# Optimization experiments

Hardware: AMD Instinct MI355X
Metric: run time of the kernel (lower is better)

The kernel has to match this reference:

```python
import jax, jax.numpy as jnp
import numpy as np

B, S, D = 2, 2048, 1024
H = 16
HD = D // H

def setup_inputs() -> dict:
    key = jax.random.key(0)
    ks = jax.random.split(key, 9)
    s = 1.0 / np.sqrt(D)
    return {
        "x": jax.random.normal(ks[0], (B, S, D), dtype=jnp.float32),
        "Wq": jax.random.normal(ks[1], (D, D), dtype=jnp.float32) * s,
        "bq": jnp.zeros((D,), dtype=jnp.float32),
        "Wk": jax.random.normal(ks[2], (D, D), dtype=jnp.float32) * s,
        "bk": jnp.zeros((D,), dtype=jnp.float32),
        "Wv": jax.random.normal(ks[3], (D, D), dtype=jnp.float32) * s,
        "bv": jnp.zeros((D,), dtype=jnp.float32),
        "Wo": jax.random.normal(ks[4], (D, D), dtype=jnp.float32) * s,
        "bo": jnp.zeros((D,), dtype=jnp.float32),
    }

def reference(x, Wq, bq, Wk, bk, Wv, bv, Wo, bo):
    b, s, d = x.shape
    # torch Linear: y = x @ W.T + b
    def proj(W, bias):
        y = jnp.einsum('bsd,ed->bse', x, W) + bias
        return y.reshape(b, s, H, HD).transpose(0, 2, 1, 3)  # [b,h,s,hd]
    Q = proj(Wq, bq)
    K = proj(Wk, bk)
    V = proj(Wv, bv)
    scale = 1.0 / jnp.sqrt(jnp.float32(HD))
    scores = jnp.einsum('bhqd,bhkd->bhqk', Q, K) * scale  # [b,h,s,s]
    attn = jax.nn.softmax(scores, axis=-1)
    out = jnp.einsum('bhqk,bhkd->bhqd', attn, V)  # [b,h,s,hd]
    out = out.transpose(0, 2, 1, 3).reshape(b, s, d)
    return jnp.einsum('bsd,ed->bse', out, Wo) + bo
```

## Files before the change

### kernel.cpp

```cpp
#include <hip/hip_runtime.h>
#include <stdint.h>


typedef __bf16 bf16x8 __attribute__((ext_vector_type(8)));
typedef float  f32x4  __attribute__((ext_vector_type(4)));

#define LOG2E 1.44269504088896f
#define FIXED_MAX_BITS 14.4269504088896f

__device__ __forceinline__ unsigned short f2bf(float f) {
    union { float f; unsigned u; } v; v.f = f;
    unsigned r = v.u + 0x7FFFu + ((v.u >> 16) & 1u);
    return (unsigned short)(r >> 16);
}
__device__ __forceinline__ float bf2f(unsigned short u) {
    union { unsigned u; float f; } v; v.u = (unsigned)u << 16; return v.f;
}

__device__ __forceinline__ float exp2_fast(float x) {
#if __has_builtin(__builtin_amdgcn_exp2f)
    return __builtin_amdgcn_exp2f(x);
#else
    return __expf(x * 0.69314718056f);
#endif
}

__device__ __forceinline__ void glds16(const void* g, void* l) {
    __builtin_amdgcn_global_load_lds(
        (__attribute__((address_space(1))) void*)(g),
        (__attribute__((address_space(3))) void*)(l),
        16, 0, 0);
}

__global__ __launch_bounds__(256) void cvt_all(
    const float* __restrict__ x,  const float* __restrict__ Wq,
    const float* __restrict__ Wk, const float* __restrict__ Wv,
    const float* __restrict__ Wo,
    unsigned short* __restrict__ xb,  unsigned short* __restrict__ Wqb,
    unsigned short* __restrict__ Wkb, unsigned short* __restrict__ Wvb,
    unsigned short* __restrict__ Wob)
{
    const int stride = gridDim.x * blockDim.x;
    for (int i = blockIdx.x * blockDim.x + threadIdx.x; i < 2097152; i += stride) {
        const float* src; unsigned short* dst; int j;
        if (i < 1048576) { src = x; dst = xb; j = i; }
        else {
            int t = (i - 1048576) >> 18; j = (i - 1048576) & 262143;
            src = (t == 0) ? Wq : (t == 1) ? Wk : (t == 2) ? Wv : Wo;
            dst = (t == 0) ? Wqb : (t == 1) ? Wkb : (t == 2) ? Wvb : Wob;
        }
        float4 v = ((const float4*)src)[j];
        ushort4 o;
        o.x = f2bf(v.x); o.y = f2bf(v.y); o.z = f2bf(v.z); o.w = f2bf(v.w);
        ((ushort4*)dst)[j] = o;
    }
}

template <int MODE>
__global__ __launch_bounds__(256) void gemm_bt(
    const unsigned short* __restrict__ A,
    const unsigned short* __restrict__ W0,
    const unsigned short* __restrict__ W1,
    const unsigned short* __restrict__ W2,
    const float* __restrict__ b0,
    const float* __restrict__ b1,
    const float* __restrict__ b2,
    unsigned short* __restrict__ outQ,
    unsigned short* __restrict__ outK,
    unsigned short* __restrict__ outV,
    float* __restrict__ outF)
{
    constexpr int BM = (MODE == 0) ? 128 : 64;
    constexpr int FM = BM / 32;
    constexpr int RA = BM / 32;

    __shared__ __attribute__((aligned(16))) unsigned short As[2 * BM * 64];
    __shared__ __attribute__((aligned(16))) unsigned short Bs[2 * 128 * 64];

    const int tid  = threadIdx.x;
    const int lane = tid & 63;
    const int wid  = tid >> 6;
    const int quad = lane >> 4;
    const int l16  = lane & 15;

    const int m0 = blockIdx.x * BM;

    const unsigned short* W;
    const float* bias;
    int proj, n0;
    if (MODE == 0) {
        proj = blockIdx.y >> 3;
        n0   = (blockIdx.y & 7) * 128;
        W    = (proj == 0) ? W0 : (proj == 1) ? W1 : W2;
        bias = (proj == 0) ? b0 : (proj == 1) ? b1 : b2;
    } else {
        proj = 0;
        n0   = blockIdx.y * 128;
        W    = W0;
        bias = b0;
    }

    const int wm = (wid >> 1) * (BM / 2);
    const int wn = (wid & 1) * 64;

    f32x4 acc[FM][4];
#pragma unroll
    for (int i = 0; i < FM; ++i)
#pragma unroll
        for (int j = 0; j < 4; ++j)
            acc[i][j] = (f32x4){0.f, 0.f, 0.f, 0.f};

    char* AsB = (char*)As;
    char* BsB = (char*)Bs;

    auto stageAB = [&](int k0, int buf) {
        char* ldsA = AsB + buf * (BM * 128) + wid * 1024;
        char* ldsB = BsB + buf * 16384 + wid * 1024;
#pragma unroll
        for (int q = 0; q < RA; ++q) {
            int i   = q * 256 + tid;
            int row = i >> 3;
            int sc  = (i & 7) ^ (row & 7);
            glds16(A + (size_t)(m0 + row) * 1024 + k0 + sc * 8, ldsA + q * 4096);
        }
#pragma unroll
        for (int q = 0; q < 4; ++q) {
            int i   = q * 256 + tid;
            int row = i >> 3;
            int sc  = (i & 7) ^ (row & 7);
            glds16(W + (size_t)(n0 + row) * 1024 + k0 + sc * 8, ldsB + q * 4096);
        }
    };

    stageAB(0, 0);
    __syncthreads();

    for (int k0 = 0; k0 < 1024; k0 += 64) {
        const int cur = (k0 >> 6) & 1;
        if (k0 + 64 < 1024) stageAB(k0 + 64, cur ^ 1);

        const char* AsC = AsB + cur * (BM * 128);
        const char* BsC = BsB + cur * 16384;

#pragma unroll
        for (int kh = 0; kh < 2; ++kh) {
            bf16x8 af[FM], bfr[4];
#pragma unroll
            for (int t = 0; t < FM; ++t) {
                int r = wm + t * 16 + l16;
                int c = (kh * 4 + quad) ^ (r & 7);
                af[t] = *(const bf16x8*)(AsC + r * 128 + c * 16);
            }
#pragma unroll
            for (int t = 0; t < 4; ++t) {
                int r = wn + t * 16 + l16;
                int c = (kh * 4 + quad) ^ (r & 7);
                bfr[t] = *(const bf16x8*)(BsC + r * 128 + c * 16);
            }
#pragma unroll
            for (int i = 0; i < FM; ++i)
#pragma unroll
                for (int j = 0; j < 4; ++j)
                    acc[i][j] = __builtin_amdgcn_mfma_f32_16x16x32_bf16(
                        af[i], bfr[j], acc[i][j], 0, 0, 0);
        }
        __syncthreads();
    }

#pragma unroll
    for (int i = 0; i < FM; ++i) {
        const int mrow0 = m0 + wm + i * 16 + quad * 4;
#pragma unroll
        for (int j = 0; j < 4; ++j) {
            const int n  = n0 + wn + j * 16 + l16;
            const float bb = bias[n];
            if (MODE == 1) {
#pragma unroll
                for (int r = 0; r < 4; ++r)
                    outF[(size_t)(mrow0 + r) * 1024 + n] = acc[i][j][r] + bb;
            } else {
                const int h = n >> 6, hd = n & 63;
                if (proj == 2) {
                    const int b = mrow0 >> 11, s = mrow0 & 2047;
                    ushort4 pk;
                    pk.x = f2bf(acc[i][j][0] + bb);
                    pk.y = f2bf(acc[i][j][1] + bb);
                    pk.z = f2bf(acc[i][j][2] + bb);
                    pk.w = f2bf(acc[i][j][3] + bb);
                    *(ushort4*)(outV + ((size_t)((b * 16 + h) * 64 + hd)) * 2048 + s) = pk;
                } else {
                    unsigned short* dst = (proj == 0) ? outQ : outK;
                    const float scl = (proj == 0) ? (0.125f * LOG2E) : 1.0f;
#pragma unroll
                    for (int r = 0; r < 4; ++r) {
                        const int m = mrow0 + r;
                        const int b = m >> 11, s = m & 2047;
                        dst[((size_t)((b * 16 + h) * 2048 + s)) * 64 + hd] =
                            f2bf((acc[i][j][r] + bb) * scl);
                    }
                }
            }
        }
    }
}

__global__ __launch_bounds__(256, 4) void attn_kernel(
    const unsigned short* __restrict__ Qb,
    const unsigned short* __restrict__ Kb,
    const unsigned short* __restrict__ Vtb,
    unsigned short* __restrict__ OP,
    float* __restrict__ LS)
{
    __shared__ __attribute__((aligned(16))) unsigned short Ks[2 * 64 * 64];
    __shared__ __attribute__((aligned(16))) unsigned short Vs[2 * 64 * 64];

    const int tid  = threadIdx.x;
    const int lane = tid & 63;
    const int wid  = tid >> 6;
    const int quad = lane >> 4;
    const int l16  = lane & 15;
    const int l7   = l16 & 7;

    const int bid  = blockIdx.x + (blockIdx.y << 5);
    const int c8   = bid & 7;
    const int t    = bid >> 3;
    const int hb   = c8 + ((t >> 5) << 3);
    const int u    = t & 31;
    const int qt16 = u >> 1;
    const int half = u & 1;
    const int q0   = qt16 * 128 + wid * 32;
    const int bq   = hb >> 4, hh = hb & 15;

    const unsigned short* Qh  = Qb  + (size_t)hb * 2048 * 64;
    const unsigned short* Kh  = Kb  + (size_t)hb * 2048 * 64;
    const unsigned short* Vth = Vtb + (size_t)hb * 64 * 2048;

    bf16x8 qf[2][2];
#pragma unroll
    for (int qt = 0; qt < 2; ++qt) {
        const unsigned short* qp = Qh + (size_t)(q0 + qt * 16 + l16) * 64 + quad * 8;
        qf[qt][0] = *(const bf16x8*)(qp);
        qf[qt][1] = *(const bf16x8*)(qp + 32);
    }

    f32x4 o[4][2];
#pragma unroll
    for (int ht = 0; ht < 4; ++ht)
#pragma unroll
        for (int qt = 0; qt < 2; ++qt)
            o[ht][qt] = (f32x4){0.f, 0.f, 0.f, 0.f};
    float lsum[2] = {0.f, 0.f};

    char* KsB = (char*)Ks;
    char* VsB = (char*)Vs;

    auto stageKV = [&](int kc, int buf) {
        char* ldsK = KsB + buf * 8192 + wid * 1024;
#pragma unroll
        for (int q = 0; q < 2; ++q) {
            int i   = q * 256 + tid;
            int row = i >> 3;
            int g   = (row & 3) | (((row >> 3) & 1) << 2);
            int ch  = (i & 7) ^ g;
            glds16(Kh + (size_t)(kc + row) * 64 + ch * 8, ldsK + q * 4096);
        }
        char* ldsV = VsB + buf * 8192 + wid * 1024;
#pragma unroll
        for (int q = 0; q < 2; ++q) {
            int i   = q * 256 + tid;
            int row = i >> 3;
            int ch  = (i & 7) ^ (row & 7);
            glds16(Vth + (size_t)row * 2048 + kc + ch * 8, ldsV + q * 4096);
        }
    };

    const int base_row = 8 * (l16 >> 2) + (l16 & 3);
    const int kp0 = ((quad) ^ l7) * 16;
    const int kp1 = ((4 + quad) ^ l7) * 16;
    const int vrow = l16 * 128;

    const int kc0 = half * 1024;
    stageKV(kc0, 0);
    __syncthreads();

    for (int kc = kc0; kc < kc0 + 1024; kc += 64) {
        const int cur = (kc >> 6) & 1;
        if (kc + 64 < kc0 + 1024) stageKV(kc + 64, cur ^ 1);

        const char* KsC = KsB + cur * 8192;
        const char* VsC = VsB + cur * 8192;

#pragma unroll
        for (int st32 = 0; st32 < 2; ++st32) {
            const char* krb = KsC + (st32 * 32 + base_row) * 128;
            bf16x8 kf00 = *(const bf16x8*)(krb + kp0);
            bf16x8 kf01 = *(const bf16x8*)(krb + kp1);
            bf16x8 kf10 = *(const bf16x8*)(krb + 512 + kp0);
            bf16x8 kf11 = *(const bf16x8*)(krb + 512 + kp1);

            const f32x4 mi = (f32x4){-FIXED_MAX_BITS, -FIXED_MAX_BITS,
                                     -FIXED_MAX_BITS, -FIXED_MAX_BITS};
            f32x4 s00 = mi, s01 = mi, s10 = mi, s11 = mi;
            s00 = __builtin_amdgcn_mfma_f32_16x16x32_bf16(kf00, qf[0][0], s00, 0, 0, 0);
            s00 = __builtin_amdgcn_mfma_f32_16x16x32_bf16(kf01, qf[0][1], s00, 0, 0, 0);
            s01 = __builtin_amdgcn_mfma_f32_16x16x32_bf16(kf10, qf[0][0], s01, 0, 0, 0);
            s01 = __builtin_amdgcn_mfma_f32_16x16x32_bf16(kf11, qf[0][1], s01, 0, 0, 0);
            s10 = __builtin_amdgcn_mfma_f32_16x16x32_bf16(kf00, qf[1][0], s10, 0, 0, 0);
            s10 = __builtin_amdgcn_mfma_f32_16x16x32_bf16(kf01, qf[1][1], s10, 0, 0, 0);
            s11 = __builtin_amdgcn_mfma_f32_16x16x32_bf16(kf10, qf[1][0], s11, 0, 0, 0);
            s11 = __builtin_amdgcn_mfma_f32_16x16x32_bf16(kf11, qf[1][1], s11, 0, 0, 0);

            bf16x8 p8[2];
#pragma unroll
            for (int qt = 0; qt < 2; ++qt) {
                const f32x4 sA = qt ? s10 : s00;
                const f32x4 sB = qt ? s11 : s01;
                float e0 = exp2_fast(sA[0]), e1 = exp2_fast(sA[1]);
                float e2 = exp2_fast(sA[2]), e3 = exp2_fast(sA[3]);
                float e4 = exp2_fast(sB[0]), e5 = exp2_fast(sB[1]);
                float e6 = exp2_fast(sB[2]), e7 = exp2_fast(sB[3]);
                lsum[qt] += ((e0 + e1) + (e2 + e3)) + ((e4 + e5) + (e6 + e7));
                bf16x8 p;
                p[0] = (__bf16)e0; p[1] = (__bf16)e1;
                p[2] = (__bf16)e2; p[3] = (__bf16)e3;
                p[4] = (__bf16)e4; p[5] = (__bf16)e5;
                p[6] = (__bf16)e6; p[7] = (__bf16)e7;
                p8[qt] = p;
            }

            const int voff = vrow + (((st32 * 4 + quad) ^ l7) * 16);
#pragma unroll
            for (int ht = 0; ht < 4; ++ht) {
                const bf16x8 vf = *(const bf16x8*)(VsC + voff + ht * 2048);
                o[ht][0] = __builtin_amdgcn_mfma_f32_16x16x32_bf16(vf, p8[0], o[ht][0], 0, 0, 0);
                o[ht][1] = __builtin_amdgcn_mfma_f32_16x16x32_bf16(vf, p8[1], o[ht][1], 0, 0, 0);
            }
        }
        __syncthreads();
    }

    float lt[2];
#pragma unroll
    for (int qt = 0; qt < 2; ++qt) {
        float s = lsum[qt];
        s += __shfl_xor(s, 16);
        s += __shfl_xor(s, 32);
        lt[qt] = s;
    }

    unsigned short* OPh = OP + (size_t)half * 4096 * 1024;
#pragma unroll
    for (int qt = 0; qt < 2; ++qt) {
        const size_t row = (size_t)(bq * 2048 + q0 + qt * 16 + l16);
#pragma unroll
        for (int ht = 0; ht < 4; ++ht) {
            ushort4 pk;
            pk.x = f2bf(o[ht][qt][0]);
            pk.y = f2bf(o[ht][qt][1]);
            pk.z = f2bf(o[ht][qt][2]);
            pk.w = f2bf(o[ht][qt][3]);
            *(ushort4*)(OPh + row * 1024 + hh * 64 + ht * 16 + quad * 4) = pk;
        }
    }
    if (quad == 0) {
        LS[half * 65536 + hb * 2048 + q0 + l16]      = lt[0];
        LS[half * 65536 + hb * 2048 + q0 + 16 + l16] = lt[1];
    }
}

__global__ __launch_bounds__(256) void attn_reduce(
    const unsigned short* __restrict__ OP,
    const float* __restrict__ LS,
    unsigned short* __restrict__ attnb)
{
    const size_t idx = ((size_t)blockIdx.x * 256 + threadIdx.x) * 8;
    const int row = (int)(idx >> 10);
    const int col = (int)(idx & 1023);
    const int bh  = ((row >> 11) << 4) + (col >> 6);
    const int q   = row & 2047;
    const float l = LS[bh * 2048 + q] + LS[65536 + bh * 2048 + q];
    const float rl = 1.0f / l;

    ushort4 a0 = *(const ushort4*)(OP + idx);
    ushort4 a1 = *(const ushort4*)(OP + idx + 4);
    ushort4 b0 = *(const ushort4*)(OP + 4194304 + idx);
    ushort4 b1 = *(const ushort4*)(OP + 4194304 + idx + 4);
    ushort4 o0, o1;
    o0.x = f2bf((bf2f(a0.x) + bf2f(b0.x)) * rl);
    o0.y = f2bf((bf2f(a0.y) + bf2f(b0.y)) * rl);
    o0.z = f2bf((bf2f(a0.z) + bf2f(b0.z)) * rl);
    o0.w = f2bf((bf2f(a0.w) + bf2f(b0.w)) * rl);
    o1.x = f2bf((bf2f(a1.x) + bf2f(b1.x)) * rl);
    o1.y = f2bf((bf2f(a1.y) + bf2f(b1.y)) * rl);
    o1.z = f2bf((bf2f(a1.z) + bf2f(b1.z)) * rl);
    o1.w = f2bf((bf2f(a1.w) + bf2f(b1.w)) * rl);
    *(ushort4*)(attnb + idx)     = o0;
    *(ushort4*)(attnb + idx + 4) = o1;
}

extern "C" void kernel_launch(void* const* d_in, const int* in_sizes, int n_in,
                              void* d_out, int out_size, void* d_ws, size_t ws_size,
                              hipStream_t stream) {
    (void)in_sizes; (void)n_in; (void)out_size; (void)ws_size;

    const float* x  = (const float*)d_in[0];
    const float* Wq = (const float*)d_in[1];
    const float* bq = (const float*)d_in[2];
    const float* Wk = (const float*)d_in[3];
    const float* bk = (const float*)d_in[4];
    const float* Wv = (const float*)d_in[5];
    const float* bv = (const float*)d_in[6];
    const float* Wo = (const float*)d_in[7];
    const float* bo = (const float*)d_in[8];

    char* ws = (char*)d_ws;
    const size_t MB = 1024 * 1024;
    unsigned short* xb    = (unsigned short*)(ws + 0);
    unsigned short* Wqb   = (unsigned short*)(ws + 8  * MB);
    unsigned short* Wkb   = (unsigned short*)(ws + 10 * MB);
    unsigned short* Wvb   = (unsigned short*)(ws + 12 * MB);
    unsigned short* Wob   = (unsigned short*)(ws + 14 * MB);
    unsigned short* Qb    = (unsigned short*)(ws + 16 * MB);
    unsigned short* Kb    = (unsigned short*)(ws + 24 * MB);
    unsigned short* Vtb   = (unsigned short*)(ws + 32 * MB);
    unsigned short* attnb = (unsigned short*)(ws + 40 * MB);
    unsigned short* OP    = (unsigned short*)(ws + 48 * MB);
    float*          LSb   = (float*)(ws + 64 * MB);

    cvt_all<<<dim3(1024), dim3(256), 0, stream>>>(
        x, Wq, Wk, Wv, Wo, xb, Wqb, Wkb, Wvb, Wob);

    gemm_bt<0><<<dim3(32, 24), dim3(256), 0, stream>>>(
        xb, Wqb, Wkb, Wvb, bq, bk, bv, Qb, Kb, Vtb, nullptr);

    attn_kernel<<<dim3(32, 32), dim3(256), 0, stream>>>(Qb, Kb, Vtb, OP, LSb);

    attn_reduce<<<dim3(2048), dim3(256), 0, stream>>>(OP, LSb, attnb);

    gemm_bt<1><<<dim3(64, 8), dim3(256), 0, stream>>>(
        attnb, Wob, nullptr, nullptr, bo, nullptr, nullptr,
        nullptr, nullptr, nullptr, (float*)d_out);
}
```

Baseline: 189.8 us.

## Fuse split-KV attention reduce into output projection GEMM A-tile loading

Removes the separate attn_reduce kernel. The output-projection GEMM now loads both partial attention outputs into registers, sums them, scales by a per-row reciprocal of the summed softmax denominators kept in shared memory, and writes bf16 into the LDS A tile, with the commit placed after the MFMAs. This drops one kernel launch and a full write and reread of the combined attention buffer. In exchange the GEMM reads twice the A data through registers instead of async global-to-LDS loads, and register pressure rises. The attention kernel's launch-bounds occupancy hint is also raised from 4 to 5.

```diff
diff --git a/kernel.cpp b/kernel.cpp
--- a/kernel.cpp
+++ b/kernel.cpp
@@ -12,9 +12,6 @@
     union { float f; unsigned u; } v; v.f = f;
     unsigned r = v.u + 0x7FFFu + ((v.u >> 16) & 1u);
     return (unsigned short)(r >> 16);
-}
-__device__ __forceinline__ float bf2f(unsigned short u) {
-    union { unsigned u; float f; } v; v.u = (unsigned)u << 16; return v.f;
 }
 
 __device__ __forceinline__ float exp2_fast(float x) {
@@ -23,6 +20,18 @@
 #else
     return __expf(x * 0.69314718056f);
 #endif
+}
+
+__device__ __forceinline__ unsigned comb2(unsigned wa, unsigned wb, float rl) {
+    union { unsigned u; float f; } la, ha, lb, hb;
+    la.u = wa << 16; ha.u = wa & 0xffff0000u;
+    lb.u = wb << 16; hb.u = wb & 0xffff0000u;
+    float lo = (la.f + lb.f) * rl;
+    float hi = (ha.f + hb.f) * rl;
+    __bf16 l = (__bf16)lo, h = (__bf16)hi;
+    unsigned short lu = __builtin_bit_cast(unsigned short, l);
+    unsigned short hu = __builtin_bit_cast(unsigned short, h);
+    return (unsigned)lu | ((unsigned)hu << 16);
 }
 
 __device__ __forceinline__ void glds16(const void* g, void* l) {
@@ -76,6 +85,7 @@
 
     __shared__ __attribute__((aligned(16))) unsigned short As[2 * BM * 64];
     __shared__ __attribute__((aligned(16))) unsigned short Bs[2 * 128 * 64];
+    __shared__ float Lrec[(MODE == 1) ? 1024 : 4];
 
     const int tid  = threadIdx.x;
     const int lane = tid & 63;
@@ -113,9 +123,18 @@
     char* AsB = (char*)As;
     char* BsB = (char*)Bs;
 
-    auto stageAB = [&](int k0, int buf) {
+    auto stageB = [&](int k0, int buf) {
+        char* ldsB = BsB + buf * 16384 + wid * 1024;
+#pragma unroll
+        for (int q = 0; q < 4; ++q) {
+            int i   = q * 256 + tid;
+            int row = i >> 3;
+            int sc  = (i & 7) ^ (row & 7);
+            glds16(W + (size_t)(n0 + row) * 1024 + k0 + sc * 8, ldsB + q * 4096);
+        }
+    };
+    auto stageA_g = [&](int k0, int buf) {
         char* ldsA = AsB + buf * (BM * 128) + wid * 1024;
-        char* ldsB = BsB + buf * 16384 + wid * 1024;
 #pragma unroll
         for (int q = 0; q < RA; ++q) {
             int i   = q * 256 + tid;
@@ -123,21 +142,68 @@
             int sc  = (i & 7) ^ (row & 7);
             glds16(A + (size_t)(m0 + row) * 1024 + k0 + sc * 8, ldsA + q * 4096);
         }
-#pragma unroll
-        for (int q = 0; q < 4; ++q) {
+    };
+
+    uint4 ar0[2], ar1[2];
+    float arl[2];
+    auto aload = [&](int k0) {
+#pragma unroll
+        for (int q = 0; q < 2; ++q) {
             int i   = q * 256 + tid;
             int row = i >> 3;
             int sc  = (i & 7) ^ (row & 7);
-            glds16(W + (size_t)(n0 + row) * 1024 + k0 + sc * 8, ldsB + q * 4096);
+            const size_t gof = (size_t)(m0 + row) * 1024 + k0 + sc * 8;
+            ar0[q] = *(const uint4*)(A + gof);
+            ar1[q] = *(const uint4*)(A + 4194304 + gof);
+            arl[q] = Lrec[row * 16 + (k0 >> 6)];
         }
     };
-
-    stageAB(0, 0);
+    auto acommit = [&](int buf) {
+#pragma unroll
+        for (int q = 0; q < 2; ++q) {
+            int i = q * 256 + tid;
+            uint4 o;
+            o.x = comb2(ar0[q].x, ar1[q].x, arl[q]);
+            o.y = comb2(ar0[q].y, ar1[q].y, arl[q]);
+            o.z = comb2(ar0[q].z, ar1[q].z, arl[q]);
+            o.w = comb2(ar0[q].w, ar1[q].w, arl[q]);
+            *(uint4*)(AsB + buf * (BM * 128) + i * 16) = o;
+        }
+    };
+
+    if constexpr (MODE == 1) {
+        const float* LSp = b1;
+        const int bq16 = (m0 >> 11) << 4;
+        const int mq0  = m0 & 2047;
+#pragma unroll
+        for (int j = 0; j < 4; ++j) {
+            int idx = j * 256 + tid;
+            int rr  = idx >> 4, h = idx & 15;
+            int off = (bq16 + h) * 2048 + mq0 + rr;
+            Lrec[idx] = 1.0f / (LSp[off] + LSp[65536 + off]);
+        }
+        __syncthreads();
+        aload(0);
+        acommit(0);
+        stageB(0, 0);
+    } else {
+        stageA_g(0, 0);
+        stageB(0, 0);
+    }
     __syncthreads();
 
     for (int k0 = 0; k0 < 1024; k0 += 64) {
         const int cur = (k0 >> 6) & 1;
-        if (k0 + 64 < 1024) stageAB(k0 + 64, cur ^ 1);
+        const bool pf = (k0 + 64 < 1024);
+        if (pf) {
+            if constexpr (MODE == 1) {
+                aload(k0 + 64);
+                stageB(k0 + 64, cur ^ 1);
+            } else {
+                stageA_g(k0 + 64, cur ^ 1);
+                stageB(k0 + 64, cur ^ 1);
+            }
+        }
 
         const char* AsC = AsB + cur * (BM * 128);
         const char* BsC = BsB + cur * 16384;
@@ -163,6 +229,10 @@
                 for (int j = 0; j < 4; ++j)
                     acc[i][j] = __builtin_amdgcn_mfma_f32_16x16x32_bf16(
                         af[i], bfr[j], acc[i][j], 0, 0, 0);
+        }
+
+        if constexpr (MODE == 1) {
+            if (pf) acommit(cur ^ 1);
         }
         __syncthreads();
     }
@@ -204,7 +274,7 @@
     }
 }
 
-__global__ __launch_bounds__(256, 4) void attn_kernel(
+__global__ __launch_bounds__(256, 5) void attn_kernel(
     const unsigned short* __restrict__ Qb,
     const unsigned short* __restrict__ Kb,
     const unsigned short* __restrict__ Vtb,
@@ -368,36 +438,6 @@
     }
 }
 
-__global__ __launch_bounds__(256) void attn_reduce(
-    const unsigned short* __restrict__ OP,
-    const float* __restrict__ LS,
-    unsigned short* __restrict__ attnb)
-{
-    const size_t idx = ((size_t)blockIdx.x * 256 + threadIdx.x) * 8;
-    const int row = (int)(idx >> 10);
-    const int col = (int)(idx & 1023);
-    const int bh  = ((row >> 11) << 4) + (col >> 6);
-    const int q   = row & 2047;
-    const float l = LS[bh * 2048 + q] + LS[65536 + bh * 2048 + q];
-    const float rl = 1.0f / l;
-
-    ushort4 a0 = *(const ushort4*)(OP + idx);
-    ushort4 a1 = *(const ushort4*)(OP + idx + 4);
-    ushort4 b0 = *(const ushort4*)(OP + 4194304 + idx);
-    ushort4 b1 = *(const ushort4*)(OP + 4194304 + idx + 4);
-    ushort4 o0, o1;
-    o0.x = f2bf((bf2f(a0.x) + bf2f(b0.x)) * rl);
-    o0.y = f2bf((bf2f(a0.y) + bf2f(b0.y)) * rl);
-    o0.z = f2bf((bf2f(a0.z) + bf2f(b0.z)) * rl);
-    o0.w = f2bf((bf2f(a0.w) + bf2f(b0.w)) * rl);
-    o1.x = f2bf((bf2f(a1.x) + bf2f(b1.x)) * rl);
-    o1.y = f2bf((bf2f(a1.y) + bf2f(b1.y)) * rl);
-    o1.z = f2bf((bf2f(a1.z) + bf2f(b1.z)) * rl);
-    o1.w = f2bf((bf2f(a1.w) + bf2f(b1.w)) * rl);
-    *(ushort4*)(attnb + idx)     = o0;
-    *(ushort4*)(attnb + idx + 4) = o1;
-}
-
 extern "C" void kernel_launch(void* const* d_in, const int* in_sizes, int n_in,
                               void* d_out, int out_size, void* d_ws, size_t ws_size,
                               hipStream_t stream) {
@@ -423,7 +463,6 @@
     unsigned short* Qb    = (unsigned short*)(ws + 16 * MB);
     unsigned short* Kb    = (unsigned short*)(ws + 24 * MB);
     unsigned short* Vtb   = (unsigned short*)(ws + 32 * MB);
-    unsigned short* attnb = (unsigned short*)(ws + 40 * MB);
     unsigned short* OP    = (unsigned short*)(ws + 48 * MB);
     float*          LSb   = (float*)(ws + 64 * MB);
 
@@ -435,9 +474,7 @@
 
     attn_kernel<<<dim3(32, 32), dim3(256), 0, stream>>>(Qb, Kb, Vtb, OP, LSb);
 
-    attn_reduce<<<dim3(2048), dim3(256), 0, stream>>>(OP, LSb, attnb);
-
     gemm_bt<1><<<dim3(64, 8), dim3(256), 0, stream>>>(
-        attnb, Wob, nullptr, nullptr, bo, nullptr, nullptr,
+        OP, Wob, nullptr, nullptr, bo, LSb, nullptr,
         nullptr, nullptr, nullptr, (float*)d_out);
 }
```

Result: slower. 259.9 us (+36.9%).
